# Kernel tuning notes

Measured on AMD Instinct MI355X. Metric: run time of the kernel, lower is better.

Reference implementation:

```python
import jax, jax.numpy as jnp
import numpy as np

D_MODEL = 1024
N_HEADS = 16
HEAD_DIM = D_MODEL // N_HEADS
B, L = 2, 2048


def setup_inputs() -> dict:
    key = jax.random.key(0)
    ks = jax.random.split(key, 9)
    s = 1.0 / np.sqrt(D_MODEL)
    return {
        "hidden_states": jax.random.normal(ks[0], (B, L, D_MODEL), dtype=jnp.float32),
        "Wq": jax.random.uniform(ks[1], (D_MODEL, D_MODEL), jnp.float32, -s, s),
        "bq": jax.random.uniform(ks[2], (D_MODEL,), jnp.float32, -s, s),
        "Wk": jax.random.uniform(ks[3], (D_MODEL, D_MODEL), jnp.float32, -s, s),
        "bk": jax.random.uniform(ks[4], (D_MODEL,), jnp.float32, -s, s),
        "Wv": jax.random.uniform(ks[5], (D_MODEL, D_MODEL), jnp.float32, -s, s),
        "bv": jax.random.uniform(ks[6], (D_MODEL,), jnp.float32, -s, s),
        "Wo": jax.random.uniform(ks[7], (D_MODEL, D_MODEL), jnp.float32, -s, s),
        "bo": jax.random.uniform(ks[8], (D_MODEL,), jnp.float32, -s, s),
    }


def reference(hidden_states, Wq, bq, Wk, bk, Wv, bv, Wo, bo):
    b, l, d = hidden_states.shape
    h, hd = N_HEADS, HEAD_DIM
    scale = jnp.sqrt(jnp.asarray(hd, hidden_states.dtype))
    # projections (weights stored as [in, out], equivalent to torch Linear W.T)
    Q = (hidden_states @ Wq + bq).reshape(b, l, h, hd).transpose(0, 2, 1, 3)
    K = (hidden_states @ Wk + bk).reshape(b, l, h, hd).transpose(0, 2, 1, 3)
    V = (hidden_states @ Wv + bv).reshape(b, l, h, hd).transpose(0, 2, 1, 3)
    # [b, h, l, l] scores with causal mask
    scores = jnp.einsum("bhqd,bhkd->bhqk", Q, K) / scale
    causal = jnp.tril(jnp.ones((l, l), dtype=bool))
    scores = jnp.where(causal, scores, jnp.asarray(-jnp.inf, scores.dtype))
    weights = jax.nn.softmax(scores, axis=-1)
    out = jnp.einsum("bhqk,bhkd->bhqd", weights, V)
    out = out.transpose(0, 2, 1, 3).reshape(b, l, d)
    return out @ Wo + bo
```

## Files before the change

### kernel.cpp

```cpp
#include <hip/hip_runtime.h>

typedef unsigned short u16;
typedef unsigned int u32;
typedef __attribute__((ext_vector_type(8))) short bf16x8;
typedef __attribute__((ext_vector_type(4))) float f32x4;

__device__ __forceinline__ u16 f2bf(float f) {
    union { float f; u32 u; } x; x.f = f;
    u32 r = x.u + 0x7FFFu + ((x.u >> 16) & 1u);
    return (u16)(r >> 16);
}

__device__ __forceinline__ u16 f2bf_fast(float f) {
    union { float f; u32 u; } x; x.f = f;
    return (u16)((x.u + 0x8000u) >> 16);
}

__device__ __forceinline__ void gload16(const u16* g, u16* l) {
    __builtin_amdgcn_global_load_lds(
        (const __attribute__((address_space(1))) void*)g,
        (__attribute__((address_space(3))) void*)l,
        16, 0, 0);
}

__device__ __forceinline__ f32x4 mfma16(bf16x8 a, bf16x8 b, f32x4 c) {
    return __builtin_amdgcn_mfma_f32_16x16x32_bf16(a, b, c, 0, 0, 0);
}


__global__ __launch_bounds__(256) void cvt_x(const float* __restrict__ in, u16* __restrict__ out, int n4) {
    int i = blockIdx.x * blockDim.x + threadIdx.x;
    if (i >= n4) return;
    float4 v = ((const float4*)in)[i];
    u16* o = out + (size_t)i * 4;
    o[0] = f2bf(v.x); o[1] = f2bf(v.y); o[2] = f2bf(v.z); o[3] = f2bf(v.w);
}

__global__ __launch_bounds__(256) void transpose_w4(const float* __restrict__ Wq, const float* __restrict__ Wk,
                                                    const float* __restrict__ Wv, const float* __restrict__ Wo,
                                                    u16* __restrict__ qkvt, u16* __restrict__ wot) {
    __shared__ float tile[32][33];
    const float* in;
    u16* out;
    if (blockIdx.z == 0)      { in = Wq; out = qkvt; }
    else if (blockIdx.z == 1) { in = Wk; out = qkvt + 1024 * 1024; }
    else if (blockIdx.z == 2) { in = Wv; out = qkvt + 2 * 1024 * 1024; }
    else                      { in = Wo; out = wot; }
    const int bx = blockIdx.x * 32, by = blockIdx.y * 32;
    const int tx = threadIdx.x & 31, ty4 = (threadIdx.x >> 5) * 4;
#pragma unroll
    for (int j = 0; j < 4; ++j)
        tile[ty4 + j][tx] = in[(size_t)(by + ty4 + j) * 1024 + bx + tx];
    __syncthreads();
#pragma unroll
    for (int j = 0; j < 4; ++j)
        out[(size_t)(bx + ty4 + j) * 1024 + by + tx] = f2bf(tile[tx][ty4 + j]);
}

__global__ __launch_bounds__(256) void pack_bias(const float* __restrict__ bq, const float* __restrict__ bk,
                                                 const float* __restrict__ bv, float* __restrict__ out) {
    int i = blockIdx.x * blockDim.x + threadIdx.x;
    if (i >= 3072) return;
    out[i] = (i < 1024) ? bq[i] : ((i < 2048) ? bk[i - 1024] : bv[i - 2048]);
}

template<int MODE>
__global__ __launch_bounds__(256) void gemm128(const u16* __restrict__ A, const u16* __restrict__ Bt,
                                               const float* __restrict__ bias,
                                               u16* __restrict__ oq, u16* __restrict__ ok, u16* __restrict__ ov,
                                               float* __restrict__ of, int K)
{
    __shared__ u16 As[128 * 64];
    __shared__ u16 Bs[128 * 64];

    const int n0 = blockIdx.x * 128;
    const int m0 = blockIdx.y * 128;
    const int t = threadIdx.x;
    const int w = t >> 6, lane = t & 63;
    const int g = lane >> 4, lr = lane & 15;
    const int wm = w >> 1, wn = w & 1;
    const int sw = lr & 7;

    const int srow = lane >> 3;
    const int schunk = (lane & 7) ^ srow;
    const u16* pA = A  + (size_t)(m0 + w * 8 + srow) * K + schunk * 8;
    const u16* pB = Bt + (size_t)(n0 + w * 8 + srow) * K + schunk * 8;
    u16* lA = &As[w * 512 + lane * 8];
    u16* lB = &Bs[w * 512 + lane * 8];

    const int sa_row = (wm * 64 + lr) * 64;
    const int sb_row = (wn * 64 + lr) * 64;

    f32x4 acc[4][4] = {};

    for (int k0 = 0; k0 < K; k0 += 64) {
        __syncthreads();
#pragma unroll
        for (int i = 0; i < 4; ++i) {
            gload16(pA + (size_t)i * 32 * K + k0, lA + i * 2048);
            gload16(pB + (size_t)i * 32 * K + k0, lB + i * 2048);
        }
        __syncthreads();
#pragma unroll
        for (int kk = 0; kk < 2; ++kk) {
            const int cofs = ((kk * 4 + g) ^ sw) * 8;
            bf16x8 af[4], bf[4];
#pragma unroll
            for (int mi = 0; mi < 4; ++mi) af[mi] = *(const bf16x8*)&As[sa_row + mi * 16 * 64 + cofs];
#pragma unroll
            for (int ni = 0; ni < 4; ++ni) bf[ni] = *(const bf16x8*)&Bs[sb_row + ni * 16 * 64 + cofs];
#pragma unroll
            for (int mi = 0; mi < 4; ++mi)
#pragma unroll
                for (int ni = 0; ni < 4; ++ni)
                    acc[mi][ni] = mfma16(af[mi], bf[ni], acc[mi][ni]);
        }
    }

#pragma unroll
    for (int mi = 0; mi < 4; ++mi) {
#pragma unroll
        for (int ni = 0; ni < 4; ++ni) {
            const int col = n0 + wn * 64 + ni * 16 + lr;
            const int row0 = m0 + wm * 64 + mi * 16 + g * 4;
            const float bs = bias[col];
            if (MODE == 0) {
                const int mat = col >> 10;
                const int nn = col & 1023;
                const int h = nn >> 6, d = nn & 63;
                const int b = row0 >> 11, ll0 = row0 & 2047;
                const int bh = b * 16 + h;
                if (mat == 0) {
#pragma unroll
                    for (int j = 0; j < 4; ++j)
                        oq[((size_t)bh * 2048 + ll0 + j) * 64 + d] =
                            f2bf((acc[mi][ni][j] + bs) * 0.1803368801111244f);
                } else if (mat == 1) {
#pragma unroll
                    for (int j = 0; j < 4; ++j)
                        ok[((size_t)bh * 2048 + ll0 + j) * 64 + d] = f2bf(acc[mi][ni][j] + bs);
                } else {
                    union { ushort4 s4; u16 u[4]; } pk;
#pragma unroll
                    for (int j = 0; j < 4; ++j) pk.u[j] = f2bf(acc[mi][ni][j] + bs);
                    *(ushort4*)&ov[((size_t)bh * 64 + d) * 2048 + ll0] = pk.s4;
                }
            } else {
#pragma unroll
                for (int j = 0; j < 4; ++j)
                    of[(size_t)(row0 + j) * 1024 + col] = acc[mi][ni][j] + bs;
            }
        }
    }
}

__global__ __launch_bounds__(256) void attn(const u16* __restrict__ Q, const u16* __restrict__ Kg,
                                            const u16* __restrict__ Vt, u16* __restrict__ O,
                                            float* __restrict__ Opart, float* __restrict__ Mp,
                                            float* __restrict__ Lp, int do_split)
{
    __shared__ u16 Ks[64 * 64];
    __shared__ u16 Vs[64 * 64];
    __shared__ u16 Ps[4][16 * 64];

    const int bh = blockIdx.x;
    int qb, k_lo, k_hi, split;
    if (!do_split) {
        qb = 31 - (int)blockIdx.y; k_lo = 0; k_hi = qb + 1; split = -1;
    } else {
        const int y = (int)blockIdx.y;
        if (y < 32) {
            qb = 16 + (y >> 1);
            split = y & 1;
            const int mid = (qb + 1) >> 1;
            k_lo = split ? mid : 0;
            k_hi = split ? qb + 1 : mid;
        } else {
            qb = 47 - y; k_lo = 0; k_hi = qb + 1; split = -1;
        }
    }
    const int q0 = qb * 64;
    const int t = threadIdx.x;
    const int w = t >> 6, lane = t & 63;
    const int g = lane >> 4, lr = lane & 15;
    const int qw = q0 + w * 16;
    const int sw = lr & 7;

    const u16* Qb = Q  + (size_t)bh * 2048 * 64;
    const u16* Kb = Kg + (size_t)bh * 2048 * 64;
    const u16* Vb = Vt + (size_t)bh * 64 * 2048;

    const bf16x8 qf0 = *(const bf16x8*)&Qb[(size_t)(qw + lr) * 64 + g * 8];
    const bf16x8 qf1 = *(const bf16x8*)&Qb[(size_t)(qw + lr) * 64 + 32 + g * 8];

    const short one = (short)0x3F80;
    const bf16x8 vones = {one, one, one, one, one, one, one, one};

    f32x4 oacc[4] = {};
    f32x4 lsacc = {};
    float mrun = -1e30f;

    int bpaddr[4];
#pragma unroll
    for (int j = 0; j < 4; ++j) bpaddr[j] = (20 * g + j) * 4;

    const int pw_base = lr * 64;
    const int g2h = g >> 1;
    const int wic2 = (2 * g) & 3;

    bf16x8 kreg[2], vreg[2];
    const int srow0 = t >> 3, sch = t & 7;
    auto issue = [&](int kb) {
#pragma unroll
        for (int i = 0; i < 2; ++i) {
            const int row = srow0 + i * 32;
            kreg[i] = *(const bf16x8*)&Kb[(size_t)(kb * 64 + row) * 64 + sch * 8];
            vreg[i] = *(const bf16x8*)&Vb[(size_t)row * 2048 + kb * 64 + sch * 8];
        }
    };
    auto commit = [&]() {
#pragma unroll
        for (int i = 0; i < 2; ++i) {
            const int row = srow0 + i * 32;
            const int chs = sch ^ (row & 7);
            *(bf16x8*)&Ks[row * 64 + chs * 8] = kreg[i];
            *(bf16x8*)&Vs[row * 64 + chs * 8] = vreg[i];
        }
    };

    issue(k_lo);

    for (int kb = k_lo; kb < k_hi; ++kb) {
        const int k0 = kb * 64;
        __syncthreads();
        commit();
        __syncthreads();
        if (kb + 1 < k_hi) issue(kb + 1);

        f32x4 s[4] = {};
        __builtin_amdgcn_s_setprio(1);
#pragma unroll
        for (int ni = 0; ni < 4; ++ni) {
            const int row = ni * 16 + lr;
            bf16x8 kf0 = *(const bf16x8*)&Ks[row * 64 + (g ^ sw) * 8];
            bf16x8 kf1 = *(const bf16x8*)&Ks[row * 64 + ((4 + g) ^ sw) * 8];
            s[ni] = mfma16(kf0, qf0, s[ni]);
            s[ni] = mfma16(kf1, qf1, s[ni]);
        }
        __builtin_amdgcn_s_setprio(0);

        if (kb == qb) {
            const int qq = qw + lr;
#pragma unroll
            for (int ni = 0; ni < 4; ++ni)
#pragma unroll
                for (int j = 0; j < 4; ++j)
                    if (k0 + ni * 16 + g * 4 + j > qq) s[ni][j] = -1e30f;
        }

        float pm = fmaxf(fmaxf(fmaxf(s[0][0], s[0][1]), fmaxf(s[0][2], s[0][3])),
                         fmaxf(fmaxf(s[1][0], s[1][1]), fmaxf(s[1][2], s[1][3])));
        pm = fmaxf(pm, fmaxf(fmaxf(fmaxf(s[2][0], s[2][1]), fmaxf(s[2][2], s[2][3])),
                             fmaxf(fmaxf(s[3][0], s[3][1]), fmaxf(s[3][2], s[3][3]))));
        pm = fmaxf(pm, __shfl_xor(pm, 16));
        pm = fmaxf(pm, __shfl_xor(pm, 32));

        if (__any(pm > mrun + 8.f)) {
            const float mn = fmaxf(mrun, pm);
            const float r = __builtin_amdgcn_exp2f(mrun - mn);
            mrun = mn;
            const int ri = __float_as_int(r);
#pragma unroll
            for (int j = 0; j < 4; ++j) {
                const float ro = __int_as_float(__builtin_amdgcn_ds_bpermute(bpaddr[j], ri));
                lsacc[j] *= ro;
#pragma unroll
                for (int df = 0; df < 4; ++df) oacc[df][j] *= ro;
            }
        }

#pragma unroll
        for (int ni = 0; ni < 4; ++ni) {
            const int c8 = 2 * ni + g2h;
#pragma unroll
            for (int jp = 0; jp < 2; ++jp) {
                const float plo = __builtin_amdgcn_exp2f(s[ni][2 * jp]     - mrun);
                const float phi = __builtin_amdgcn_exp2f(s[ni][2 * jp + 1] - mrun);
                const u32 pr = (u32)f2bf_fast(plo) | ((u32)f2bf_fast(phi) << 16);
                const int wic = wic2 + jp;
                *(u32*)&Ps[w][pw_base + (c8 ^ sw) * 8 + wic * 2] = pr;
            }
        }

        const bf16x8 p0 = *(const bf16x8*)&Ps[w][lr * 64 + (g ^ sw) * 8];
        const bf16x8 p1 = *(const bf16x8*)&Ps[w][lr * 64 + ((4 + g) ^ sw) * 8];
        __builtin_amdgcn_s_setprio(1);
        lsacc = mfma16(p0, vones, lsacc);
        lsacc = mfma16(p1, vones, lsacc);
#pragma unroll
        for (int df = 0; df < 4; ++df) {
            const int row = df * 16 + lr;
            bf16x8 vf0 = *(const bf16x8*)&Vs[row * 64 + (g ^ sw) * 8];
            bf16x8 vf1 = *(const bf16x8*)&Vs[row * 64 + ((4 + g) ^ sw) * 8];
            oacc[df] = mfma16(p0, vf0, oacc[df]);
            oacc[df] = mfma16(p1, vf1, oacc[df]);
        }
        __builtin_amdgcn_s_setprio(0);
    }

    if (split < 0) {
        const int b = bh >> 4, h = bh & 15;
#pragma unroll
        for (int j = 0; j < 4; ++j) {
            const float inv = 1.f / lsacc[j];
            const int l = qw + g * 4 + j;
#pragma unroll
            for (int df = 0; df < 4; ++df)
                O[((size_t)b * 2048 + l) * 1024 + h * 64 + df * 16 + lr] = f2bf(oacc[df][j] * inv);
        }
    } else {
        float* Ob = Opart + ((size_t)split * 32 + bh) * (1024 * 64);
        const int rb = qw - 1024 + 4 * g;
#pragma unroll
        for (int j = 0; j < 4; ++j)
#pragma unroll
            for (int df = 0; df < 4; ++df)
                Ob[(size_t)(rb + j) * 64 + df * 16 + lr] = oacc[df][j];
        if (lr == 0) {
#pragma unroll
            for (int j = 0; j < 4; ++j)
                Lp[(split * 32 + bh) * 1024 + rb + j] = lsacc[j];
        }
        if (g == 0)
            Mp[(split * 32 + bh) * 1024 + (qw - 1024) + lr] = mrun;
    }
}

__global__ __launch_bounds__(256) void attn_merge(const float* __restrict__ Opart,
                                                  const float* __restrict__ Mp,
                                                  const float* __restrict__ Lp,
                                                  u16* __restrict__ O)
{
    const int idx = blockIdx.x * 256 + threadIdx.x;
    const int d  = idx & 63;
    const int rr = (idx >> 6) & 1023;
    const int bh = idx >> 16;
    const int si = bh * 1024 + rr;
    const float m0 = Mp[si], m1 = Mp[32 * 1024 + si];
    const float l0 = Lp[si], l1 = Lp[32 * 1024 + si];
    const float M  = fmaxf(m0, m1);
    const float w0 = __builtin_amdgcn_exp2f(m0 - M);
    const float w1 = __builtin_amdgcn_exp2f(m1 - M);
    const float o0 = Opart[(size_t)si * 64 + d];
    const float o1 = Opart[(size_t)(32 * 1024 + si) * 64 + d];
    const float o  = (w0 * o0 + w1 * o1) / (w0 * l0 + w1 * l1);
    const int b = bh >> 4, h = bh & 15;
    const int r = 1024 + rr;
    O[((size_t)b * 2048 + r) * 1024 + h * 64 + d] = f2bf(o);
}


extern "C" void kernel_launch(void* const* d_in, const int* in_sizes, int n_in,
                              void* d_out, int out_size, void* d_ws, size_t ws_size,
                              hipStream_t stream)
{
    const float* hs = (const float*)d_in[0];
    const float* Wq = (const float*)d_in[1];
    const float* bq = (const float*)d_in[2];
    const float* Wk = (const float*)d_in[3];
    const float* bk = (const float*)d_in[4];
    const float* Wv = (const float*)d_in[5];
    const float* bv = (const float*)d_in[6];
    const float* Wo = (const float*)d_in[7];
    const float* bo = (const float*)d_in[8];
    float* out = (float*)d_out;

    char* ws = (char*)d_ws;
    u16*   Xbf   = (u16*)(ws);
    u16*   Wqkvt = (u16*)(ws + (8ull  << 20));
    u16*   Wot   = (u16*)(ws + (14ull << 20));
    float* bqkv  = (float*)(ws + (16ull << 20));
    u16*   Qbuf  = (u16*)(ws + (17ull << 20));
    u16*   Kbuf  = (u16*)(ws + (25ull << 20));
    u16*   Vtbuf = (u16*)(ws + (33ull << 20));
    u16*   Abuf  = Xbf;
    float* Opart = (float*)(ws + (42ull << 20));
    float* Mpart = (float*)(ws + (58ull << 20));
    float* Lpart = (float*)(ws + (58ull << 20) + (512ull << 10));

    const int do_split = (ws_size >= (59ull << 20)) ? 1 : 0;

    cvt_x<<<4096, 256, 0, stream>>>(hs, Xbf, 4096 * 1024 / 4);
    transpose_w4<<<dim3(32, 32, 4), 256, 0, stream>>>(Wq, Wk, Wv, Wo, Wqkvt, Wot);
    pack_bias<<<12, 256, 0, stream>>>(bq, bk, bv, bqkv);

    gemm128<0><<<dim3(24, 32), 256, 0, stream>>>(Xbf, Wqkvt, bqkv, Qbuf, Kbuf, Vtbuf, nullptr, 1024);

    if (do_split) {
        attn<<<dim3(32, 48), 256, 0, stream>>>(Qbuf, Kbuf, Vtbuf, Abuf, Opart, Mpart, Lpart, 1);
        attn_merge<<<8192, 256, 0, stream>>>(Opart, Mpart, Lpart, Abuf);
    } else {
        attn<<<dim3(32, 32), 256, 0, stream>>>(Qbuf, Kbuf, Vtbuf, Abuf, nullptr, nullptr, nullptr, 0);
    }

    gemm128<1><<<dim3(8, 32), 256, 0, stream>>>(Abuf, Wot, bo, nullptr, nullptr, nullptr, out, 1024);
}
```

Baseline: 123.8 us.

## Use graded 2/3/4-way KV splits for causal attention and store partials as bf16

Replaces the fixed two-way KV split for the upper half of query blocks with a graded scheme. Blocks 10-19 split 2 ways, 20-29 split 3 ways and 30-31 split 4 ways, while the first 10 blocks run unsplit. This balances per-workgroup work across the causal triangle and raises the workgroup count. Partial outputs are normalized and stored as bf16 instead of fp32 to cut merge traffic, and the merge kernel reweights a variable number of slices. The cost is more merge work and an extra bf16 rounding of the partials.

```diff
diff --git a/kernel.cpp b/kernel.cpp
--- a/kernel.cpp
+++ b/kernel.cpp
@@ -14,6 +14,10 @@
 __device__ __forceinline__ u16 f2bf_fast(float f) {
     union { float f; u32 u; } x; x.f = f;
     return (u16)((x.u + 0x8000u) >> 16);
+}
+
+__device__ __forceinline__ float bf2f(u16 v) {
+    union { u32 u; float f; } x; x.u = (u32)v << 16; return x.f;
 }
 
 __device__ __forceinline__ void gload16(const u16* g, u16* l) {
@@ -156,7 +160,7 @@
 
 __global__ __launch_bounds__(256) void attn(const u16* __restrict__ Q, const u16* __restrict__ Kg,
                                             const u16* __restrict__ Vt, u16* __restrict__ O,
-                                            float* __restrict__ Opart, float* __restrict__ Mp,
+                                            u16* __restrict__ Opart, float* __restrict__ Mp,
                                             float* __restrict__ Lp, int do_split)
 {
     __shared__ u16 Ks[64 * 64];
@@ -164,19 +168,21 @@
     __shared__ u16 Ps[4][16 * 64];
 
     const int bh = blockIdx.x;
-    int qb, k_lo, k_hi, split;
+    int qb, k_lo, k_hi, slot;
     if (!do_split) {
-        qb = 31 - (int)blockIdx.y; k_lo = 0; k_hi = qb + 1; split = -1;
+        qb = 31 - (int)blockIdx.y; k_lo = 0; k_hi = qb + 1; slot = -1;
     } else {
         const int y = (int)blockIdx.y;
-        if (y < 32) {
-            qb = 16 + (y >> 1);
-            split = y & 1;
-            const int mid = (qb + 1) >> 1;
-            k_lo = split ? mid : 0;
-            k_hi = split ? qb + 1 : mid;
+        if (y < 10) {
+            qb = 9 - y; k_lo = 0; k_hi = qb + 1; slot = -1;
         } else {
-            qb = 47 - y; k_lo = 0; k_hi = qb + 1; split = -1;
+            slot = 67 - y;
+            int c, S;
+            if (slot < 20)      { qb = 10 + (slot >> 1);       c = slot & 1;        S = 2; }
+            else if (slot < 50) { qb = 20 + (slot - 20) / 3;   c = (slot - 20) % 3; S = 3; }
+            else                { qb = 30 + ((slot - 50) >> 2); c = (slot - 50) & 3; S = 4; }
+            k_lo = c * (qb + 1) / S;
+            k_hi = (c + 1) * (qb + 1) / S;
         }
     }
     const int q0 = qb * 64;
@@ -308,7 +314,7 @@
         __builtin_amdgcn_s_setprio(0);
     }
 
-    if (split < 0) {
+    if (slot < 0) {
         const int b = bh >> 4, h = bh & 15;
 #pragma unroll
         for (int j = 0; j < 4; ++j) {
@@ -319,44 +325,49 @@
                 O[((size_t)b * 2048 + l) * 1024 + h * 64 + df * 16 + lr] = f2bf(oacc[df][j] * inv);
         }
     } else {
-        float* Ob = Opart + ((size_t)split * 32 + bh) * (1024 * 64);
-        const int rb = qw - 1024 + 4 * g;
-#pragma unroll
-        for (int j = 0; j < 4; ++j)
+        u16* Ob = Opart + ((size_t)(bh * 58 + slot) << 12);
+        const int rbase = w * 16 + g * 4;
+#pragma unroll
+        for (int j = 0; j < 4; ++j) {
+            const float inv = 1.f / lsacc[j];
+            const int r = rbase + j;
 #pragma unroll
             for (int df = 0; df < 4; ++df)
-                Ob[(size_t)(rb + j) * 64 + df * 16 + lr] = oacc[df][j];
-        if (lr == 0) {
-#pragma unroll
-            for (int j = 0; j < 4; ++j)
-                Lp[(split * 32 + bh) * 1024 + rb + j] = lsacc[j];
-        }
-        if (g == 0)
-            Mp[(split * 32 + bh) * 1024 + (qw - 1024) + lr] = mrun;
-    }
-}
-
-__global__ __launch_bounds__(256) void attn_merge(const float* __restrict__ Opart,
+                Ob[r * 64 + df * 16 + lr] = f2bf(oacc[df][j] * inv);
+            if (lr == 0) Lp[(bh * 58 + slot) * 64 + r] = lsacc[j];
+        }
+        if (g == 0) Mp[(bh * 58 + slot) * 64 + w * 16 + lr] = mrun;
+    }
+}
+
+__global__ __launch_bounds__(256) void attn_merge(const u16* __restrict__ Opart,
                                                   const float* __restrict__ Mp,
                                                   const float* __restrict__ Lp,
                                                   u16* __restrict__ O)
 {
     const int idx = blockIdx.x * 256 + threadIdx.x;
-    const int d  = idx & 63;
-    const int rr = (idx >> 6) & 1023;
-    const int bh = idx >> 16;
-    const int si = bh * 1024 + rr;
-    const float m0 = Mp[si], m1 = Mp[32 * 1024 + si];
-    const float l0 = Lp[si], l1 = Lp[32 * 1024 + si];
-    const float M  = fmaxf(m0, m1);
-    const float w0 = __builtin_amdgcn_exp2f(m0 - M);
-    const float w1 = __builtin_amdgcn_exp2f(m1 - M);
-    const float o0 = Opart[(size_t)si * 64 + d];
-    const float o1 = Opart[(size_t)(32 * 1024 + si) * 64 + d];
-    const float o  = (w0 * o0 + w1 * o1) / (w0 * l0 + w1 * l1);
+    const int d = idx & 63;
+    const int t2 = idx >> 6;
+    const int bh = t2 / 1408;
+    const int row = 640 + (t2 - bh * 1408);
+    const int qb = row >> 6;
+    int base, S;
+    if (qb < 20)      { base = (qb - 10) * 2;        S = 2; }
+    else if (qb < 30) { base = 20 + (qb - 20) * 3;   S = 3; }
+    else              { base = 50 + (qb - 30) * 4;   S = 4; }
+    const int r = row & 63;
+    const int sbase = (bh * 58 + base) * 64 + r;
+
+    float M = -1e30f;
+    for (int i = 0; i < S; ++i) M = fmaxf(M, Mp[sbase + i * 64]);
+    float num = 0.f, den = 0.f;
+    for (int i = 0; i < S; ++i) {
+        const float wi = __builtin_amdgcn_exp2f(Mp[sbase + i * 64] - M) * Lp[sbase + i * 64];
+        den += wi;
+        num += wi * bf2f(Opart[(((size_t)(bh * 58 + base + i)) << 12) + r * 64 + d]);
+    }
     const int b = bh >> 4, h = bh & 15;
-    const int r = 1024 + rr;
-    O[((size_t)b * 2048 + r) * 1024 + h * 64 + d] = f2bf(o);
+    O[((size_t)b * 2048 + row) * 1024 + h * 64 + d] = f2bf(num / den);
 }
 
 
@@ -384,8 +395,8 @@
     u16*   Kbuf  = (u16*)(ws + (25ull << 20));
     u16*   Vtbuf = (u16*)(ws + (33ull << 20));
     u16*   Abuf  = Xbf;
-    float* Opart = (float*)(ws + (42ull << 20));
-    float* Mpart = (float*)(ws + (58ull << 20));
+    u16*   Opart = (u16*)(ws + (42ull << 20));
+    float* Mpart = (float*)(ws + (57ull << 20) + (512ull << 10));
     float* Lpart = (float*)(ws + (58ull << 20) + (512ull << 10));
 
     const int do_split = (ws_size >= (59ull << 20)) ? 1 : 0;
@@ -397,8 +408,8 @@
     gemm128<0><<<dim3(24, 32), 256, 0, stream>>>(Xbf, Wqkvt, bqkv, Qbuf, Kbuf, Vtbuf, nullptr, 1024);
 
     if (do_split) {
-        attn<<<dim3(32, 48), 256, 0, stream>>>(Qbuf, Kbuf, Vtbuf, Abuf, Opart, Mpart, Lpart, 1);
-        attn_merge<<<8192, 256, 0, stream>>>(Opart, Mpart, Lpart, Abuf);
+        attn<<<dim3(32, 68), 256, 0, stream>>>(Qbuf, Kbuf, Vtbuf, Abuf, Opart, Mpart, Lpart, 1);
+        attn_merge<<<11264, 256, 0, stream>>>(Opart, Mpart, Lpart, Abuf);
     } else {
         attn<<<dim3(32, 32), 256, 0, stream>>>(Qbuf, Kbuf, Vtbuf, Abuf, nullptr, nullptr, nullptr, 0);
     }
```

After: 132.7 us. +7.3%, slower.
